# Kernel tuning notes

Hardware: AMD Instinct MI355X
Metric: run time of the kernel (lower is better)

The kernel has to match this reference:

```python
import jax, jax.numpy as jnp
import numpy as np

NEG_SLOPE = 0.2
EPS = 1e-16  # PyG softmax denominator epsilon

N_NODES = 50000
N_EDGES = 800000
IN_CH = 128
HID = 64
HEADS = 4


def setup_inputs() -> dict:
    key = jax.random.key(0)
    ks = jax.random.split(key, 10)
    rng = np.random.default_rng(0)
    src = rng.integers(0, N_NODES, N_EDGES)
    dst = rng.integers(0, N_NODES, N_EDGES)
    dst = np.where(src == dst, (dst + 1) % N_NODES, dst)  # no pre-existing self-loops
    edge_index = jnp.asarray(np.stack([src, dst]), dtype=jnp.int32)
    s = 0.1
    return {
        "x": jax.random.normal(ks[0], (N_NODES, IN_CH), jnp.float32),
        "edge_index": edge_index,
        "W1": jax.random.normal(ks[1], (IN_CH, HEADS * HID), jnp.float32) * s,
        "att_src1": jax.random.normal(ks[2], (HEADS, HID), jnp.float32) * s,
        "att_dst1": jax.random.normal(ks[3], (HEADS, HID), jnp.float32) * s,
        "b1": jnp.zeros((HEADS * HID,), jnp.float32),
        "W2": jax.random.normal(ks[4], (HEADS * HID, HID), jnp.float32) * s,
        "att_src2": jax.random.normal(ks[5], (1, HID), jnp.float32) * s,
        "att_dst2": jax.random.normal(ks[6], (1, HID), jnp.float32) * s,
        "b2": jnp.zeros((HID,), jnp.float32),
    }


def _gat_conv(x, src, dst, W, att_src, att_dst, bias, heads, out_ch, concat):
    """PyG GATConv: messages flow src -> dst, softmax over edges sharing dst."""
    n = x.shape[0]
    h = (x @ W).reshape(n, heads, out_ch)                  # [N,H,C]
    a_s = jnp.einsum('nhc,hc->nh', h, att_src)             # [N,H]
    a_d = jnp.einsum('nhc,hc->nh', h, att_dst)             # [N,H]
    e = jax.nn.leaky_relu(a_s[src] + a_d[dst], NEG_SLOPE)  # [E,H]
    e_max = jax.ops.segment_max(e, dst, num_segments=n)
    e_max = jnp.where(jnp.isfinite(e_max), e_max, 0.0)
    ex = jnp.exp(e - e_max[dst])                           # [E,H]
    denom = jax.ops.segment_sum(ex, dst, num_segments=n)   # [N,H]
    alpha = ex / (denom[dst] + EPS)                        # [E,H]
    msg = h[src] * alpha[:, :, None]                       # [E,H,C]
    out = jax.ops.segment_sum(msg, dst, num_segments=n)    # [N,H,C]
    if concat:
        out = out.reshape(n, heads * out_ch)
    else:
        out = out.mean(axis=1)
    return out + bias


def reference(x, edge_index, W1, att_src1, att_dst1, b1, W2, att_src2, att_dst2, b2):
    n = x.shape[0]
    loops = jnp.arange(n, dtype=edge_index.dtype)
    src = jnp.concatenate([edge_index[0], loops])  # GATConv add_self_loops=True
    dst = jnp.concatenate([edge_index[1], loops])
    h = _gat_conv(x, src, dst, W1, att_src1, att_dst1, b1, HEADS, HID, True)
    h = jax.nn.elu(h)
    h = _gat_conv(h, src, dst, W2, att_src2, att_dst2, b2, 1, HID, False)
    node_u = h[edge_index[0]]
    node_v = h[edge_index[1]]
    return jnp.concatenate([node_u, node_v], axis=-1)  # [E, 2*HID]
```

## Files before the change

kernel.cpp:

```cpp
#include <hip/hip_runtime.h>
#include <hip/hip_bf16.h>

#define NEG_SLOPE 0.2f
#define EPS 1e-16f

typedef short  bf16x8  __attribute__((ext_vector_type(8)));
typedef float  f32x4   __attribute__((ext_vector_type(4)));
typedef float  nfloat4 __attribute__((ext_vector_type(4)));

__device__ __forceinline__ float bf2f(unsigned short u) {
    union { unsigned int i; float f; } c; c.i = ((unsigned int)u) << 16; return c.f;
}
__device__ __forceinline__ ushort f2bf(float f) {
    __hip_bfloat16 b = __float2bfloat16(f);
    return *(ushort*)&b;
}

__global__ void hist_k(const int* __restrict__ dst, int E, int* __restrict__ deg) {
    int e = blockIdx.x * blockDim.x + threadIdx.x;
    if (e < E) atomicAdd(&deg[dst[e]], 1);
}

__global__ __launch_bounds__(1024) void scan1_k(const int* __restrict__ deg, int* __restrict__ offs,
                                                int* __restrict__ bsum, int n) {
    __shared__ int tmp[1024];
    int t = threadIdx.x;
    int i = blockIdx.x * 1024 + t;
    int v = (i < n) ? deg[i] : 0;
    tmp[t] = v;
    __syncthreads();
    int run = v;
    for (int off = 1; off < 1024; off <<= 1) {
        int add = (t >= off) ? tmp[t - off] : 0;
        __syncthreads();
        run += add;
        tmp[t] = run;
        __syncthreads();
    }
    if (i < n) offs[i] = run - v;
    if (t == 1023) bsum[blockIdx.x] = run;
}

__global__ void scan2_k(int* bsum, int nb) {
    if (blockIdx.x == 0 && threadIdx.x == 0) {
        int acc = 0;
        for (int i = 0; i < nb; i++) { int v = bsum[i]; bsum[i] = acc; acc += v; }
    }
}

__global__ __launch_bounds__(1024) void scan3_k(int* __restrict__ offs, const int* __restrict__ bsum,
                                                int n, int total) {
    int i = blockIdx.x * 1024 + threadIdx.x;
    if (i < n) offs[i] += bsum[blockIdx.x];
    if (i == 0) offs[n] = total;
}

__global__ void fill_k(const int* __restrict__ src, const int* __restrict__ dst, int E,
                       const int* __restrict__ offs, int* __restrict__ cur, int* __restrict__ csr) {
    int e = blockIdx.x * blockDim.x + threadIdx.x;
    if (e >= E) return;
    int d = dst[e];
    int pos = offs[d] + atomicAdd(&cur[d], 1);
    csr[pos] = src[e];
}

__global__ void convx_k(const float4* __restrict__ xv, ushort4* __restrict__ xhi4,
                        ushort4* __restrict__ xlo4, int n4) {
    int t = blockIdx.x * blockDim.x + threadIdx.x;
    if (t >= n4) return;
    float4 v = xv[t];
    ushort4 h, l;
    h.x = f2bf(v.x); l.x = f2bf(v.x - bf2f(h.x));
    h.y = f2bf(v.y); l.y = f2bf(v.y - bf2f(h.y));
    h.z = f2bf(v.z); l.z = f2bf(v.z - bf2f(h.z));
    h.w = f2bf(v.w); l.w = f2bf(v.w - bf2f(h.w));
    xhi4[t] = h; xlo4[t] = l;
}

__global__ void wprep1_k(const float* __restrict__ W1, const float* __restrict__ attS,
                         const float* __restrict__ attD, ushort* __restrict__ bhi,
                         ushort* __restrict__ blo) {
    int tid = blockIdx.x * blockDim.x + threadIdx.x;
    if (tid >= 17 * 4 * 64 * 8) return;
    int j = tid & 7, lane = (tid >> 3) & 63, ks = (tid >> 9) & 3, nt = tid >> 11;
    int k = ks * 32 + (lane >> 4) * 8 + j;
    int col = nt * 16 + (lane & 15);
    float v = 0.f;
    if (col < 256) v = W1[k * 256 + col];
    else if (col < 264) {
        int cc = col - 256, h = cc & 3;
        const float* att = (cc < 4) ? attS : attD;
        float s = 0.f;
        for (int c = 0; c < 64; c++) s += W1[k * 256 + h * 64 + c] * att[h * 64 + c];
        v = s;
    }
    ushort hi = f2bf(v);
    float rem = v - bf2f(hi);
    int idx = ((nt * 4 + ks) * 64 + lane) * 8 + j;
    bhi[idx] = hi; blo[idx] = f2bf(rem);
}

__global__ void wprep2_k(const float* __restrict__ W2, const float* __restrict__ attS,
                         const float* __restrict__ attD, ushort* __restrict__ bhi,
                         ushort* __restrict__ blo) {
    int tid = blockIdx.x * blockDim.x + threadIdx.x;
    if (tid >= 5 * 8 * 64 * 8) return;
    int j = tid & 7, lane = (tid >> 3) & 63, ks = (tid >> 9) & 7, nt = tid >> 12;
    int k = ks * 32 + (lane >> 4) * 8 + j;
    int col = nt * 16 + (lane & 15);
    float v = 0.f;
    if (col < 64) v = W2[k * 64 + col];
    else if (col == 64) { float s = 0.f; for (int c = 0; c < 64; c++) s += W2[k * 64 + c] * attS[c]; v = s; }
    else if (col == 65) { float s = 0.f; for (int c = 0; c < 64; c++) s += W2[k * 64 + c] * attD[c]; v = s; }
    ushort hi = f2bf(v);
    float rem = v - bf2f(hi);
    int idx = ((nt * 8 + ks) * 64 + lane) * 8 + j;
    bhi[idx] = hi; blo[idx] = f2bf(rem);
}

__global__ __launch_bounds__(256) void gemm1_mfma_k(const ushort* __restrict__ xhi, const ushort* __restrict__ xlo,
                                                    const bf16x8* __restrict__ bhi, const bf16x8* __restrict__ blo,
                                                    ushort* __restrict__ h1b, float* __restrict__ as1,
                                                    float* __restrict__ ad1, int N) {
    __shared__ ushort hs[4][16][256];
    int wid = threadIdx.x >> 6, lane = threadIdx.x & 63;
    int m0 = (blockIdx.x * 4 + wid) * 16;
    if (m0 >= N) return;
    int row = lane & 15, grp = lane >> 4;
    const bf16x8* xhi8 = (const bf16x8*)xhi;
    const bf16x8* xlo8 = (const bf16x8*)xlo;
    bf16x8 ah[4], al[4];
    size_t rb = (size_t)(m0 + row) * 16 + grp;
#pragma unroll
    for (int ks = 0; ks < 4; ks++) { ah[ks] = xhi8[rb + ks * 4]; al[ks] = xlo8[rb + ks * 4]; }

    for (int nt = 0; nt < 17; nt++) {
        f32x4 acc = {0.f, 0.f, 0.f, 0.f};
#pragma unroll
        for (int ks = 0; ks < 4; ks++) {
            bf16x8 bh = bhi[(nt * 4 + ks) * 64 + lane];
            bf16x8 bl = blo[(nt * 4 + ks) * 64 + lane];
            acc = __builtin_amdgcn_mfma_f32_16x16x32_bf16(ah[ks], bh, acc, 0, 0, 0);
            acc = __builtin_amdgcn_mfma_f32_16x16x32_bf16(al[ks], bh, acc, 0, 0, 0);
            acc = __builtin_amdgcn_mfma_f32_16x16x32_bf16(ah[ks], bl, acc, 0, 0, 0);
        }
        if (nt < 16) {
            int col = nt * 16 + row, head = col >> 6, c = col & 63;
#pragma unroll
            for (int r = 0; r < 4; r++) hs[wid][grp * 4 + r][c * 4 + head] = f2bf(acc[r]);
        } else if (row < 8) {
#pragma unroll
            for (int r = 0; r < 4; r++) {
                int node = m0 + grp * 4 + r;
                if (row < 4) as1[node * 4 + row] = acc[r];
                else         ad1[node * 4 + (row - 4)] = acc[r];
            }
        }
    }
    ushort4* dst = (ushort4*)h1b + (size_t)m0 * 64;
    const ushort4* s4 = (const ushort4*)&hs[wid][0][0];
    for (int i = lane; i < 1024; i += 64) dst[i] = s4[i];
}

__global__ __launch_bounds__(256) void gemm2_mfma_k(const ushort* __restrict__ h1e,
                                                    const bf16x8* __restrict__ bhi, const bf16x8* __restrict__ blo,
                                                    ushort* __restrict__ h2b, float* __restrict__ as2,
                                                    float* __restrict__ ad2, int N) {
    __shared__ ushort hs[4][16][64];
    int wid = threadIdx.x >> 6, lane = threadIdx.x & 63;
    int m0 = (blockIdx.x * 4 + wid) * 16;
    if (m0 >= N) return;
    int row = lane & 15, grp = lane >> 4;
    const bf16x8* a8 = (const bf16x8*)h1e;
    bf16x8 a[8];
    size_t rb = (size_t)(m0 + row) * 32 + grp;
#pragma unroll
    for (int ks = 0; ks < 8; ks++) a[ks] = a8[rb + ks * 4];

    for (int nt = 0; nt < 5; nt++) {
        f32x4 acc = {0.f, 0.f, 0.f, 0.f};
#pragma unroll
        for (int ks = 0; ks < 8; ks++) {
            bf16x8 bh = bhi[(nt * 8 + ks) * 64 + lane];
            bf16x8 bl = blo[(nt * 8 + ks) * 64 + lane];
            acc = __builtin_amdgcn_mfma_f32_16x16x32_bf16(a[ks], bh, acc, 0, 0, 0);
            acc = __builtin_amdgcn_mfma_f32_16x16x32_bf16(a[ks], bl, acc, 0, 0, 0);
        }
        if (nt < 4) {
            int col = nt * 16 + row;
#pragma unroll
            for (int r = 0; r < 4; r++) hs[wid][grp * 4 + r][col] = f2bf(acc[r]);
        } else if (row < 2) {
#pragma unroll
            for (int r = 0; r < 4; r++) {
                int node = m0 + grp * 4 + r;
                if (row == 0) as2[node] = acc[r];
                else          ad2[node] = acc[r];
            }
        }
    }
    ushort4* dst = (ushort4*)h2b + (size_t)m0 * 16;
    const ushort4* s4 = (const ushort4*)&hs[wid][0][0];
    for (int i = lane; i < 256; i += 64) dst[i] = s4[i];
}

__global__ __launch_bounds__(256) void agg4_k(const ushort4* __restrict__ hb, const float4* __restrict__ asv,
                                              const float4* __restrict__ adv, const int* __restrict__ offs,
                                              const int* __restrict__ csr, const float* __restrict__ bias,
                                              ushort* __restrict__ out, int N) {
    int node = (int)(((size_t)blockIdx.x * blockDim.x + threadIdx.x) >> 6);
    int lane = threadIdx.x & 63;
    if (node >= N) return;
    int beg = offs[node], end = offs[node + 1];
    int total = end - beg + 1;
    float4 ad = adv[node];

    float den0 = 0.f, den1 = 0.f, den2 = 0.f, den3 = 0.f;
    float acc0 = 0.f, acc1 = 0.f, acc2 = 0.f, acc3 = 0.f;

    for (int base = 0; base < total; base += 64) {
        int i = base + lane;
        bool valid = i < total;
        int s = node;
        if (valid && i > 0) s = csr[beg + i - 1];
        float4 av = asv[s];
        float e0 = av.x + ad.x; e0 = e0 > 0.f ? e0 : NEG_SLOPE * e0;
        float e1 = av.y + ad.y; e1 = e1 > 0.f ? e1 : NEG_SLOPE * e1;
        float e2 = av.z + ad.z; e2 = e2 > 0.f ? e2 : NEG_SLOPE * e2;
        float e3 = av.w + ad.w; e3 = e3 > 0.f ? e3 : NEG_SLOPE * e3;
        float p0 = valid ? __expf(e0) : 0.f;
        float p1 = valid ? __expf(e1) : 0.f;
        float p2 = valid ? __expf(e2) : 0.f;
        float p3 = valid ? __expf(e3) : 0.f;
        float q0 = p0, q1 = p1, q2 = p2, q3 = p3;
#pragma unroll
        for (int off = 32; off >= 1; off >>= 1) {
            q0 += __shfl_xor(q0, off);
            q1 += __shfl_xor(q1, off);
            q2 += __shfl_xor(q2, off);
            q3 += __shfl_xor(q3, off);
        }
        den0 += q0; den1 += q1; den2 += q2; den3 += q3;

        int cn = total - base; if (cn > 64) cn = 64;
        int cn4 = (cn + 3) & ~3;
        for (int j = 0; j < cn4; j += 4) {
            int s0 = __shfl(s, j), s1 = __shfl(s, j + 1), s2 = __shfl(s, j + 2), s3 = __shfl(s, j + 3);
            ushort4 v0 = hb[(size_t)s0 * 64 + lane];
            ushort4 v1 = hb[(size_t)s1 * 64 + lane];
            ushort4 v2 = hb[(size_t)s2 * 64 + lane];
            ushort4 v3 = hb[(size_t)s3 * 64 + lane];
            float w00 = __shfl(p0, j), w01 = __shfl(p1, j), w02 = __shfl(p2, j), w03 = __shfl(p3, j);
            acc0 = fmaf(bf2f(v0.x), w00, acc0);
            acc1 = fmaf(bf2f(v0.y), w01, acc1);
            acc2 = fmaf(bf2f(v0.z), w02, acc2);
            acc3 = fmaf(bf2f(v0.w), w03, acc3);
            float w10 = __shfl(p0, j + 1), w11 = __shfl(p1, j + 1), w12 = __shfl(p2, j + 1), w13 = __shfl(p3, j + 1);
            acc0 = fmaf(bf2f(v1.x), w10, acc0);
            acc1 = fmaf(bf2f(v1.y), w11, acc1);
            acc2 = fmaf(bf2f(v1.z), w12, acc2);
            acc3 = fmaf(bf2f(v1.w), w13, acc3);
            float w20 = __shfl(p0, j + 2), w21 = __shfl(p1, j + 2), w22 = __shfl(p2, j + 2), w23 = __shfl(p3, j + 2);
            acc0 = fmaf(bf2f(v2.x), w20, acc0);
            acc1 = fmaf(bf2f(v2.y), w21, acc1);
            acc2 = fmaf(bf2f(v2.z), w22, acc2);
            acc3 = fmaf(bf2f(v2.w), w23, acc3);
            float w30 = __shfl(p0, j + 3), w31 = __shfl(p1, j + 3), w32 = __shfl(p2, j + 3), w33 = __shfl(p3, j + 3);
            acc0 = fmaf(bf2f(v3.x), w30, acc0);
            acc1 = fmaf(bf2f(v3.y), w31, acc1);
            acc2 = fmaf(bf2f(v3.z), w32, acc2);
            acc3 = fmaf(bf2f(v3.w), w33, acc3);
        }
    }

    ushort* op = out + (size_t)node * 256 + lane;
    float o;
    o = acc0 / (den0 + EPS) + bias[lane];        o = o > 0.f ? o : expm1f(o); op[0]   = f2bf(o);
    o = acc1 / (den1 + EPS) + bias[64 + lane];   o = o > 0.f ? o : expm1f(o); op[64]  = f2bf(o);
    o = acc2 / (den2 + EPS) + bias[128 + lane];  o = o > 0.f ? o : expm1f(o); op[128] = f2bf(o);
    o = acc3 / (den3 + EPS) + bias[192 + lane];  o = o > 0.f ? o : expm1f(o); op[192] = f2bf(o);
}

__global__ __launch_bounds__(256) void agg1_k(const ushort* __restrict__ h2b, const float* __restrict__ asv,
                                              const float* __restrict__ adv, const int* __restrict__ offs,
                                              const int* __restrict__ csr, const float* __restrict__ bias,
                                              float* __restrict__ out, int N) {
    int node = (int)(((size_t)blockIdx.x * blockDim.x + threadIdx.x) >> 6);
    int lane = threadIdx.x & 63;
    if (node >= N) return;
    int beg = offs[node], end = offs[node + 1];
    int total = end - beg + 1;
    float ad = adv[node];

    float den = 0.f, acc = 0.f;
    for (int base = 0; base < total; base += 64) {
        int i = base + lane;
        bool valid = i < total;
        int s = node;
        if (valid && i > 0) s = csr[beg + i - 1];
        float e = asv[s] + ad;
        e = e > 0.f ? e : NEG_SLOPE * e;
        float p = valid ? __expf(e) : 0.f;
        float q = p;
#pragma unroll
        for (int off = 32; off >= 1; off >>= 1) q += __shfl_xor(q, off);
        den += q;

        int cn = total - base; if (cn > 64) cn = 64;
        int cn4 = (cn + 3) & ~3;
        for (int j = 0; j < cn4; j += 4) {
            int s0 = __shfl(s, j), s1 = __shfl(s, j + 1), s2 = __shfl(s, j + 2), s3 = __shfl(s, j + 3);
            float h0 = bf2f(h2b[(size_t)s0 * 64 + lane]);
            float h1 = bf2f(h2b[(size_t)s1 * 64 + lane]);
            float h2v = bf2f(h2b[(size_t)s2 * 64 + lane]);
            float h3 = bf2f(h2b[(size_t)s3 * 64 + lane]);
            acc = fmaf(h0, __shfl(p, j), acc);
            acc = fmaf(h1, __shfl(p, j + 1), acc);
            acc = fmaf(h2v, __shfl(p, j + 2), acc);
            acc = fmaf(h3, __shfl(p, j + 3), acc);
        }
    }
    out[(size_t)node * 64 + lane] = acc / (den + EPS) + bias[lane];
}

__global__ void gather_k(const nfloat4* __restrict__ h2a4, const int* __restrict__ srcv,
                         const int* __restrict__ dstv, nfloat4* __restrict__ out, int E) {
    int t = blockIdx.x * blockDim.x + threadIdx.x;
    if (t >= E * 32) return;
    int e = t >> 5, q = t & 31;
    int node = (q < 16) ? srcv[e] : dstv[e];
    nfloat4 v = h2a4[(size_t)node * 16 + (q & 15)];
    __builtin_nontemporal_store(v, &out[t]);
}

extern "C" void kernel_launch(void* const* d_in, const int* in_sizes, int n_in,
                              void* d_out, int out_size, void* d_ws, size_t ws_size,
                              hipStream_t stream) {
    const float* x   = (const float*)d_in[0];
    const int*   ei  = (const int*)d_in[1];
    const float* W1  = (const float*)d_in[2];
    const float* aS1 = (const float*)d_in[3];
    const float* aD1 = (const float*)d_in[4];
    const float* b1  = (const float*)d_in[5];
    const float* W2  = (const float*)d_in[6];
    const float* aS2 = (const float*)d_in[7];
    const float* aD2 = (const float*)d_in[8];
    const float* b2  = (const float*)d_in[9];
    float* out = (float*)d_out;

    int N = in_sizes[0] / 128;
    int E = in_sizes[1] / 2;
    const int* srcv = ei;
    const int* dstv = ei + E;

    size_t off = 0;
    char* base = (char*)d_ws;
    auto alloc = [&](size_t bytes) -> void* {
        void* p = base + off;
        off = (off + bytes + 255) & ~(size_t)255;
        return p;
    };
    int*    deg  = (int*)alloc((size_t)N * 4);
    int*    cur  = (int*)alloc((size_t)N * 4);
    int*    offs = (int*)alloc((size_t)(N + 1) * 4);
    int*    bsum = (int*)alloc(256 * 4);
    int*    csr  = (int*)alloc((size_t)E * 4);
    float*  as1  = (float*)alloc((size_t)N * 16);
    float*  ad1  = (float*)alloc((size_t)N * 16);
    float*  as2  = (float*)alloc((size_t)N * 4);
    float*  ad2  = (float*)alloc((size_t)N * 4);
    ushort* b1hi = (ushort*)alloc(17 * 4 * 64 * 8 * 2);
    ushort* b1lo = (ushort*)alloc(17 * 4 * 64 * 8 * 2);
    ushort* b2hi = (ushort*)alloc(5 * 8 * 64 * 8 * 2);
    ushort* b2lo = (ushort*)alloc(5 * 8 * 64 * 8 * 2);
    ushort* xhi  = (ushort*)alloc((size_t)N * 128 * 2);
    ushort* xlo  = (ushort*)alloc((size_t)N * 128 * 2);
    ushort* h1b  = (ushort*)alloc((size_t)N * 256 * 2);
    ushort* h1e  = xhi;
    ushort* h2b  = h1b;
    float*  h2a  = (float*)(h1b + (size_t)N * 64);

    (void)hipMemsetAsync(deg, 0, (size_t)N * 4, stream);
    (void)hipMemsetAsync(cur, 0, (size_t)N * 4, stream);

    int nbE = (E + 255) / 256;
    hist_k<<<nbE, 256, 0, stream>>>(dstv, E, deg);
    int nbS = (N + 1023) / 1024;
    scan1_k<<<nbS, 1024, 0, stream>>>(deg, offs, bsum, N);
    scan2_k<<<1, 64, 0, stream>>>(bsum, nbS);
    scan3_k<<<nbS, 1024, 0, stream>>>(offs, bsum, N, E);
    fill_k<<<nbE, 256, 0, stream>>>(srcv, dstv, E, offs, cur, csr);

    int n4 = N * 32;
    convx_k<<<(n4 + 255) / 256, 256, 0, stream>>>((const float4*)x, (ushort4*)xhi, (ushort4*)xlo, n4);
    wprep1_k<<<(17 * 4 * 64 * 8 + 255) / 256, 256, 0, stream>>>(W1, aS1, aD1, b1hi, b1lo);
    wprep2_k<<<(5 * 8 * 64 * 8 + 255) / 256, 256, 0, stream>>>(W2, aS2, aD2, b2hi, b2lo);

    int nstrip = (N + 15) / 16;
    int nbG1 = (nstrip + 3) / 4;
    gemm1_mfma_k<<<nbG1, 256, 0, stream>>>(xhi, xlo, (const bf16x8*)b1hi, (const bf16x8*)b1lo,
                                           h1b, as1, ad1, N);

    int nbA = (N * 64 + 255) / 256;
    agg4_k<<<nbA, 256, 0, stream>>>((const ushort4*)h1b, (const float4*)as1, (const float4*)ad1,
                                    offs, csr, b1, h1e, N);

    gemm2_mfma_k<<<nbG1, 256, 0, stream>>>(h1e, (const bf16x8*)b2hi, (const bf16x8*)b2lo,
                                           h2b, as2, ad2, N);

    agg1_k<<<nbA, 256, 0, stream>>>(h2b, as2, ad2, offs, csr, b2, h2a, N);

    int nbGth = (E * 32 + 255) / 256;
    gather_k<<<nbGth, 256, 0, stream>>>((const nfloat4*)h2a, srcv, dstv, (nfloat4*)out, E);
}
```

Measured before the change: 362.7 us.

## Fuse x bf16 split into GEMM1, merge weight prep, scatter output by node

The x hi/lo bf16 split now happens inside the first GEMM kernel, which removes the convx pass and its intermediate buffers. The two weight-prep kernels are merged into one launch. A second CSR keyed by source/destination node is built alongside the dst CSR, so the final gather becomes a per-node scatter: each node's feature row is read once and written to every edge slot that references it. This trades random reads of h2 for scattered nontemporal writes and adds extra atomics and slab storage in histogram/fill.

Result: slower. 496.8 us (+37.0%).

```diff
diff --git a/kernel.cpp b/kernel.cpp
--- a/kernel.cpp
+++ b/kernel.cpp
@@ -16,9 +16,14 @@
     return *(ushort*)&b;
 }
 
-__global__ void hist_k(const int* __restrict__ dst, int E, int* __restrict__ deg) {
+__global__ void hist2_k(const int* __restrict__ src, const int* __restrict__ dst, int E,
+                        int* __restrict__ deg2, int N) {
     int e = blockIdx.x * blockDim.x + threadIdx.x;
-    if (e < E) atomicAdd(&deg[dst[e]], 1);
+    if (e >= E) return;
+    int s = src[e], d = dst[e];
+    atomicAdd(&deg2[d], 1);
+    atomicAdd(&deg2[N + s], 1);
+    atomicAdd(&deg2[N + d], 1);
 }
 
 __global__ __launch_bounds__(1024) void scan1_k(const int* __restrict__ deg, int* __restrict__ offs,
@@ -55,70 +60,60 @@
     if (i == 0) offs[n] = total;
 }
 
-__global__ void fill_k(const int* __restrict__ src, const int* __restrict__ dst, int E,
-                       const int* __restrict__ offs, int* __restrict__ cur, int* __restrict__ csr) {
+__global__ void fill2_k(const int* __restrict__ src, const int* __restrict__ dst, int E,
+                        const int* __restrict__ offs, int* __restrict__ cur2,
+                        int* __restrict__ slab, int N) {
     int e = blockIdx.x * blockDim.x + threadIdx.x;
     if (e >= E) return;
-    int d = dst[e];
-    int pos = offs[d] + atomicAdd(&cur[d], 1);
-    csr[pos] = src[e];
-}
-
-__global__ void convx_k(const float4* __restrict__ xv, ushort4* __restrict__ xhi4,
-                        ushort4* __restrict__ xlo4, int n4) {
-    int t = blockIdx.x * blockDim.x + threadIdx.x;
-    if (t >= n4) return;
-    float4 v = xv[t];
-    ushort4 h, l;
-    h.x = f2bf(v.x); l.x = f2bf(v.x - bf2f(h.x));
-    h.y = f2bf(v.y); l.y = f2bf(v.y - bf2f(h.y));
-    h.z = f2bf(v.z); l.z = f2bf(v.z - bf2f(h.z));
-    h.w = f2bf(v.w); l.w = f2bf(v.w - bf2f(h.w));
-    xhi4[t] = h; xlo4[t] = l;
-}
-
-__global__ void wprep1_k(const float* __restrict__ W1, const float* __restrict__ attS,
-                         const float* __restrict__ attD, ushort* __restrict__ bhi,
-                         ushort* __restrict__ blo) {
+    int s = src[e], d = dst[e];
+    int p1 = offs[d] + atomicAdd(&cur2[d], 1);
+    slab[p1] = s;
+    int p2 = offs[N + s] + atomicAdd(&cur2[N + s], 1);
+    slab[p2] = (e << 1);
+    int p3 = offs[N + d] + atomicAdd(&cur2[N + d], 1);
+    slab[p3] = (e << 1) | 1;
+}
+
+__global__ void wprep_k(const float* __restrict__ W1, const float* __restrict__ aS1,
+                        const float* __restrict__ aD1, const float* __restrict__ W2,
+                        const float* __restrict__ aS2, const float* __restrict__ aD2,
+                        ushort* __restrict__ b1hi, ushort* __restrict__ b1lo,
+                        ushort* __restrict__ b2hi, ushort* __restrict__ b2lo) {
     int tid = blockIdx.x * blockDim.x + threadIdx.x;
-    if (tid >= 17 * 4 * 64 * 8) return;
-    int j = tid & 7, lane = (tid >> 3) & 63, ks = (tid >> 9) & 3, nt = tid >> 11;
-    int k = ks * 32 + (lane >> 4) * 8 + j;
-    int col = nt * 16 + (lane & 15);
-    float v = 0.f;
-    if (col < 256) v = W1[k * 256 + col];
-    else if (col < 264) {
-        int cc = col - 256, h = cc & 3;
-        const float* att = (cc < 4) ? attS : attD;
-        float s = 0.f;
-        for (int c = 0; c < 64; c++) s += W1[k * 256 + h * 64 + c] * att[h * 64 + c];
-        v = s;
-    }
-    ushort hi = f2bf(v);
-    float rem = v - bf2f(hi);
-    int idx = ((nt * 4 + ks) * 64 + lane) * 8 + j;
-    bhi[idx] = hi; blo[idx] = f2bf(rem);
-}
-
-__global__ void wprep2_k(const float* __restrict__ W2, const float* __restrict__ attS,
-                         const float* __restrict__ attD, ushort* __restrict__ bhi,
-                         ushort* __restrict__ blo) {
-    int tid = blockIdx.x * blockDim.x + threadIdx.x;
-    if (tid >= 5 * 8 * 64 * 8) return;
-    int j = tid & 7, lane = (tid >> 3) & 63, ks = (tid >> 9) & 7, nt = tid >> 12;
-    int k = ks * 32 + (lane >> 4) * 8 + j;
-    int col = nt * 16 + (lane & 15);
-    float v = 0.f;
-    if (col < 64) v = W2[k * 64 + col];
-    else if (col == 64) { float s = 0.f; for (int c = 0; c < 64; c++) s += W2[k * 64 + c] * attS[c]; v = s; }
-    else if (col == 65) { float s = 0.f; for (int c = 0; c < 64; c++) s += W2[k * 64 + c] * attD[c]; v = s; }
-    ushort hi = f2bf(v);
-    float rem = v - bf2f(hi);
-    int idx = ((nt * 8 + ks) * 64 + lane) * 8 + j;
-    bhi[idx] = hi; blo[idx] = f2bf(rem);
-}
-
-__global__ __launch_bounds__(256) void gemm1_mfma_k(const ushort* __restrict__ xhi, const ushort* __restrict__ xlo,
+    const int N1 = 17 * 4 * 64 * 8;
+    const int N2 = 5 * 8 * 64 * 8;
+    if (tid < N1) {
+        int j = tid & 7, lane = (tid >> 3) & 63, ks = (tid >> 9) & 3, nt = tid >> 11;
+        int k = ks * 32 + (lane >> 4) * 8 + j;
+        int col = nt * 16 + (lane & 15);
+        float v = 0.f;
+        if (col < 256) v = W1[k * 256 + col];
+        else if (col < 264) {
+            int cc = col - 256, h = cc & 3;
+            const float* att = (cc < 4) ? aS1 : aD1;
+            float s = 0.f;
+            for (int c = 0; c < 64; c++) s += W1[k * 256 + h * 64 + c] * att[h * 64 + c];
+            v = s;
+        }
+        ushort hi = f2bf(v);
+        int idx = ((nt * 4 + ks) * 64 + lane) * 8 + j;
+        b1hi[idx] = hi; b1lo[idx] = f2bf(v - bf2f(hi));
+    } else if (tid < N1 + N2) {
+        int t2 = tid - N1;
+        int j = t2 & 7, lane = (t2 >> 3) & 63, ks = (t2 >> 9) & 7, nt = t2 >> 12;
+        int k = ks * 32 + (lane >> 4) * 8 + j;
+        int col = nt * 16 + (lane & 15);
+        float v = 0.f;
+        if (col < 64) v = W2[k * 64 + col];
+        else if (col == 64) { float s = 0.f; for (int c = 0; c < 64; c++) s += W2[k * 64 + c] * aS2[c]; v = s; }
+        else if (col == 65) { float s = 0.f; for (int c = 0; c < 64; c++) s += W2[k * 64 + c] * aD2[c]; v = s; }
+        ushort hi = f2bf(v);
+        int idx = ((nt * 8 + ks) * 64 + lane) * 8 + j;
+        b2hi[idx] = hi; b2lo[idx] = f2bf(v - bf2f(hi));
+    }
+}
+
+__global__ __launch_bounds__(256) void gemm1_mfma_k(const float* __restrict__ x,
                                                     const bf16x8* __restrict__ bhi, const bf16x8* __restrict__ blo,
                                                     ushort* __restrict__ h1b, float* __restrict__ as1,
                                                     float* __restrict__ ad1, int N) {
@@ -127,13 +122,24 @@
     int m0 = (blockIdx.x * 4 + wid) * 16;
     if (m0 >= N) return;
     int row = lane & 15, grp = lane >> 4;
-    const bf16x8* xhi8 = (const bf16x8*)xhi;
-    const bf16x8* xlo8 = (const bf16x8*)xlo;
+    int rr = (m0 + row < N) ? (m0 + row) : (N - 1);
+    const float4* xrow = (const float4*)(x + (size_t)rr * 128);
+
     bf16x8 ah[4], al[4];
-    size_t rb = (size_t)(m0 + row) * 16 + grp;
-#pragma unroll
-    for (int ks = 0; ks < 4; ks++) { ah[ks] = xhi8[rb + ks * 4]; al[ks] = xlo8[rb + ks * 4]; }
-
+#pragma unroll
+    for (int ks = 0; ks < 4; ks++) {
+        float4 f0 = xrow[ks * 8 + grp * 2];
+        float4 f1 = xrow[ks * 8 + grp * 2 + 1];
+        float fv[8] = {f0.x, f0.y, f0.z, f0.w, f1.x, f1.y, f1.z, f1.w};
+#pragma unroll
+        for (int j = 0; j < 8; j++) {
+            ushort hi = f2bf(fv[j]);
+            ah[ks][j] = (short)hi;
+            al[ks][j] = (short)f2bf(fv[j] - bf2f(hi));
+        }
+    }
+
+    int rows = N - m0; if (rows > 16) rows = 16;
     for (int nt = 0; nt < 17; nt++) {
         f32x4 acc = {0.f, 0.f, 0.f, 0.f};
 #pragma unroll
@@ -152,14 +158,16 @@
 #pragma unroll
             for (int r = 0; r < 4; r++) {
                 int node = m0 + grp * 4 + r;
-                if (row < 4) as1[node * 4 + row] = acc[r];
-                else         ad1[node * 4 + (row - 4)] = acc[r];
+                if (node < N) {
+                    if (row < 4) as1[node * 4 + row] = acc[r];
+                    else         ad1[node * 4 + (row - 4)] = acc[r];
+                }
             }
         }
     }
     ushort4* dst = (ushort4*)h1b + (size_t)m0 * 64;
     const ushort4* s4 = (const ushort4*)&hs[wid][0][0];
-    for (int i = lane; i < 1024; i += 64) dst[i] = s4[i];
+    for (int i = lane; i < rows * 64; i += 64) dst[i] = s4[i];
 }
 
 __global__ __launch_bounds__(256) void gemm2_mfma_k(const ushort* __restrict__ h1e,
@@ -173,10 +181,12 @@
     int row = lane & 15, grp = lane >> 4;
     const bf16x8* a8 = (const bf16x8*)h1e;
     bf16x8 a[8];
-    size_t rb = (size_t)(m0 + row) * 32 + grp;
+    int rr = (m0 + row < N) ? (m0 + row) : (N - 1);
+    size_t rb = (size_t)rr * 32 + grp;
 #pragma unroll
     for (int ks = 0; ks < 8; ks++) a[ks] = a8[rb + ks * 4];
 
+    int rows = N - m0; if (rows > 16) rows = 16;
     for (int nt = 0; nt < 5; nt++) {
         f32x4 acc = {0.f, 0.f, 0.f, 0.f};
 #pragma unroll
@@ -194,14 +204,16 @@
 #pragma unroll
             for (int r = 0; r < 4; r++) {
                 int node = m0 + grp * 4 + r;
-                if (row == 0) as2[node] = acc[r];
-                else          ad2[node] = acc[r];
+                if (node < N) {
+                    if (row == 0) as2[node] = acc[r];
+                    else          ad2[node] = acc[r];
+                }
             }
         }
     }
     ushort4* dst = (ushort4*)h2b + (size_t)m0 * 16;
     const ushort4* s4 = (const ushort4*)&hs[wid][0][0];
-    for (int i = lane; i < 256; i += 64) dst[i] = s4[i];
+    for (int i = lane; i < rows * 16; i += 64) dst[i] = s4[i];
 }
 
 __global__ __launch_bounds__(256) void agg4_k(const ushort4* __restrict__ hb, const float4* __restrict__ asv,
@@ -323,14 +335,20 @@
     out[(size_t)node * 64 + lane] = acc / (den + EPS) + bias[lane];
 }
 
-__global__ void gather_k(const nfloat4* __restrict__ h2a4, const int* __restrict__ srcv,
-                         const int* __restrict__ dstv, nfloat4* __restrict__ out, int E) {
-    int t = blockIdx.x * blockDim.x + threadIdx.x;
-    if (t >= E * 32) return;
-    int e = t >> 5, q = t & 31;
-    int node = (q < 16) ? srcv[e] : dstv[e];
-    nfloat4 v = h2a4[(size_t)node * 16 + (q & 15)];
-    __builtin_nontemporal_store(v, &out[t]);
+__global__ __launch_bounds__(256) void gather2_k(const nfloat4* __restrict__ h2a4, const int* __restrict__ offs,
+                                                 const int* __restrict__ slab, nfloat4* __restrict__ out4,
+                                                 int N) {
+    int node = (int)(((size_t)blockIdx.x * blockDim.x + threadIdx.x) >> 6);
+    int lane = threadIdx.x & 63;
+    if (node >= N) return;
+    int beg = offs[N + node], end = offs[N + node + 1];
+    if (beg == end) return;
+    nfloat4 v = h2a4[(size_t)node * 16 + (lane & 15)];
+    for (int b = beg + (lane >> 4); b < end; b += 4) {
+        int ent = slab[b];
+        int eid = ent >> 1, role = ent & 1;
+        __builtin_nontemporal_store(v, &out4[(size_t)eid * 32 + role * 16 + (lane & 15)]);
+    }
 }
 
 extern "C" void kernel_launch(void* const* d_in, const int* in_sizes, int n_in,
@@ -360,11 +378,11 @@
         off = (off + bytes + 255) & ~(size_t)255;
         return p;
     };
-    int*    deg  = (int*)alloc((size_t)N * 4);
-    int*    cur  = (int*)alloc((size_t)N * 4);
-    int*    offs = (int*)alloc((size_t)(N + 1) * 4);
+    int*    deg2 = (int*)alloc((size_t)4 * N * 4);
+    int*    cur2 = deg2 + 2 * (size_t)N;
+    int*    offs = (int*)alloc((size_t)(2 * N + 1) * 4);
     int*    bsum = (int*)alloc(256 * 4);
-    int*    csr  = (int*)alloc((size_t)E * 4);
+    int*    slab = (int*)alloc((size_t)3 * E * 4);
     float*  as1  = (float*)alloc((size_t)N * 16);
     float*  ad1  = (float*)alloc((size_t)N * 16);
     float*  as2  = (float*)alloc((size_t)N * 4);
@@ -373,43 +391,38 @@
     ushort* b1lo = (ushort*)alloc(17 * 4 * 64 * 8 * 2);
     ushort* b2hi = (ushort*)alloc(5 * 8 * 64 * 8 * 2);
     ushort* b2lo = (ushort*)alloc(5 * 8 * 64 * 8 * 2);
-    ushort* xhi  = (ushort*)alloc((size_t)N * 128 * 2);
-    ushort* xlo  = (ushort*)alloc((size_t)N * 128 * 2);
     ushort* h1b  = (ushort*)alloc((size_t)N * 256 * 2);
-    ushort* h1e  = xhi;
+    ushort* h1e  = (ushort*)alloc((size_t)N * 256 * 2);
     ushort* h2b  = h1b;
     float*  h2a  = (float*)(h1b + (size_t)N * 64);
 
-    (void)hipMemsetAsync(deg, 0, (size_t)N * 4, stream);
-    (void)hipMemsetAsync(cur, 0, (size_t)N * 4, stream);
+    (void)hipMemsetAsync(deg2, 0, (size_t)4 * N * 4, stream);
 
     int nbE = (E + 255) / 256;
-    hist_k<<<nbE, 256, 0, stream>>>(dstv, E, deg);
-    int nbS = (N + 1023) / 1024;
-    scan1_k<<<nbS, 1024, 0, stream>>>(deg, offs, bsum, N);
+    hist2_k<<<nbE, 256, 0, stream>>>(srcv, dstv, E, deg2, N);
+    int n2 = 2 * N;
+    int nbS = (n2 + 1023) / 1024;
+    scan1_k<<<nbS, 1024, 0, stream>>>(deg2, offs, bsum, n2);
     scan2_k<<<1, 64, 0, stream>>>(bsum, nbS);
-    scan3_k<<<nbS, 1024, 0, stream>>>(offs, bsum, N, E);
-    fill_k<<<nbE, 256, 0, stream>>>(srcv, dstv, E, offs, cur, csr);
-
-    int n4 = N * 32;
-    convx_k<<<(n4 + 255) / 256, 256, 0, stream>>>((const float4*)x, (ushort4*)xhi, (ushort4*)xlo, n4);
-    wprep1_k<<<(17 * 4 * 64 * 8 + 255) / 256, 256, 0, stream>>>(W1, aS1, aD1, b1hi, b1lo);
-    wprep2_k<<<(5 * 8 * 64 * 8 + 255) / 256, 256, 0, stream>>>(W2, aS2, aD2, b2hi, b2lo);
+    scan3_k<<<nbS, 1024, 0, stream>>>(offs, bsum, n2, 3 * E);
+    fill2_k<<<nbE, 256, 0, stream>>>(srcv, dstv, E, offs, cur2, slab, N);
+
+    wprep_k<<<(17 * 4 * 64 * 8 + 5 * 8 * 64 * 8 + 255) / 256, 256, 0, stream>>>(
+        W1, aS1, aD1, W2, aS2, aD2, b1hi, b1lo, b2hi, b2lo);
 
     int nstrip = (N + 15) / 16;
     int nbG1 = (nstrip + 3) / 4;
-    gemm1_mfma_k<<<nbG1, 256, 0, stream>>>(xhi, xlo, (const bf16x8*)b1hi, (const bf16x8*)b1lo,
+    gemm1_mfma_k<<<nbG1, 256, 0, stream>>>(x, (const bf16x8*)b1hi, (const bf16x8*)b1lo,
                                            h1b, as1, ad1, N);
 
     int nbA = (N * 64 + 255) / 256;
     agg4_k<<<nbA, 256, 0, stream>>>((const ushort4*)h1b, (const float4*)as1, (const float4*)ad1,
-                                    offs, csr, b1, h1e, N);
+                                    offs, slab, b1, h1e, N);
 
     gemm2_mfma_k<<<nbG1, 256, 0, stream>>>(h1e, (const bf16x8*)b2hi, (const bf16x8*)b2lo,
                                            h2b, as2, ad2, N);
 
-    agg1_k<<<nbA, 256, 0, stream>>>(h2b, as2, ad2, offs, csr, b2, h2a, N);
-
-    int nbGth = (E * 32 + 255) / 256;
-    gather_k<<<nbGth, 256, 0, stream>>>((const nfloat4*)h2a, srcv, dstv, (nfloat4*)out, E);
-}
+    agg1_k<<<nbA, 256, 0, stream>>>(h2b, as2, ad2, offs, slab, b2, h2a, N);
+
+    gather2_k<<<nbA, 256, 0, stream>>>((const nfloat4*)h2a, offs, slab, (nfloat4*)out, N);
+}
```
